# Performance work log

Hardware: AMD Instinct MI355X
Metric: run time of the kernel (lower is better)

The kernel has to match this reference:

```python
import jax, jax.numpy as jnp
import numpy as np

N = 50000
E = 800000
IN_C, HID_C, OUT_C = 5, 64, 32


def setup_inputs() -> dict:
    key = jax.random.key(0)
    ks = jax.random.split(key, 9)
    x = jax.random.normal(ks[0], (N, IN_C), dtype=jnp.float32)
    edge_index = jax.random.randint(ks[1], (2, E), 0, N, dtype=jnp.int64)
    # SAGEConv params: lin_l (neighbor path, has bias), lin_r (root path, no bias)
    def lin(k, fan_out, fan_in):
        s = 1.0 / np.sqrt(fan_in)
        return jax.random.uniform(k, (fan_out, fan_in), jnp.float32, -s, s)
    W1l = lin(ks[2], HID_C, IN_C); b1 = jnp.zeros((HID_C,), jnp.float32); W1r = lin(ks[3], HID_C, IN_C)
    W2l = lin(ks[4], HID_C, HID_C); b2 = jnp.zeros((HID_C,), jnp.float32); W2r = lin(ks[5], HID_C, HID_C)
    W3l = lin(ks[6], OUT_C, HID_C); b3 = jnp.zeros((OUT_C,), jnp.float32); W3r = lin(ks[7], OUT_C, HID_C)
    return {"x": x, "edge_index": edge_index,
            "W1l": W1l, "b1": b1, "W1r": W1r,
            "W2l": W2l, "b2": b2, "W2r": W2r,
            "W3l": W3l, "b3": b3, "W3r": W3r}


def _sage_conv(x, src, dst, inv_deg, Wl, bl, Wr):
    # PyG SAGEConv (aggr='mean'): out = lin_l(mean_j x_j) + lin_r(x)
    msg = x[src]                                          # [E, d_in] gather
    agg = jax.ops.segment_sum(msg, dst, num_segments=N)   # [N, d_in] scatter-add
    mean = agg * inv_deg                                  # mean aggregation
    return mean @ Wl.T + bl + x @ Wr.T


def reference(x, edge_index, W1l, b1, W1r, W2l, b2, W2r, W3l, b3, W3r):
    src, dst = edge_index[0], edge_index[1]
    deg = jax.ops.segment_sum(jnp.ones((E,), x.dtype), dst, num_segments=N)
    inv_deg = (1.0 / jnp.maximum(deg, 1.0))[:, None]      # [N, 1]
    h = jax.nn.relu(_sage_conv(x, src, dst, inv_deg, W1l, b1, W1r))
    # F.dropout(p=0.2, training=self.training): identity in eval mode
    h = jax.nn.relu(_sage_conv(h, src, dst, inv_deg, W2l, b2, W2r))
    out = _sage_conv(h, src, dst, inv_deg, W3l, b3, W3r)
    return out
```

## Files before the change

kernel.cpp:

```cpp
#include <hip/hip_runtime.h>
#include <hip/hip_fp16.h>


#define N_NODES 50000
#define N_EDGES 800000
#define IN_C 5
#define HID_C 64
#define OUT_C 32

#define NB 196
#define BCAP 6144
#define BWG 800
#define BCH (N_EDGES / BWG)

typedef __attribute__((ext_vector_type(8))) short bf16x8;
typedef __attribute__((ext_vector_type(4))) float f32x4;

__device__ __forceinline__ int rfl(int v) { return __builtin_amdgcn_readfirstlane(v); }
__device__ __forceinline__ float lanebc(float v, int l) {
    return __int_as_float(__builtin_amdgcn_readlane(__float_as_int(v), l));
}
__device__ __forceinline__ unsigned short f2bf(float f) {
    unsigned u = __float_as_uint(f);
    return (unsigned short)((u + 0x7fffu + ((u >> 16) & 1u)) >> 16);
}
__device__ __forceinline__ float bf2f(unsigned short b) {
    return __uint_as_float(((unsigned)b) << 16);
}
__device__ __forceinline__ float2 unpk_h2(unsigned u) {
    __half2 h = *(__half2*)&u;
    return __half22float2(h);
}


__global__ __launch_bounds__(256) void k_prep(
    const float* __restrict__ W2l, const float* __restrict__ W2r,
    const float* __restrict__ W3l, const float* __restrict__ W3r,
    unsigned short* __restrict__ W2hi, unsigned short* __restrict__ W2lo,
    unsigned short* __restrict__ W3zhi, unsigned short* __restrict__ W3zlo,
    int* __restrict__ gcur) {
    if (blockIdx.x == 0 && threadIdx.x < NB) gcur[threadIdx.x] = 0;
    const int t = blockIdx.x * 256 + threadIdx.x;
    const int stride = gridDim.x * 256;
    for (int p = t; p < 64 * 128; p += stride) {
        int j = p >> 7, k = p & 127;
        float w = (k < 64) ? W2l[j * 64 + k] : W2r[j * 64 + (k - 64)];
        unsigned short h = f2bf(w);
        W2hi[p] = h;
        W2lo[p] = f2bf(w - bf2f(h));
    }
    for (int p = t; p < 64 * 64; p += stride) {
        int j = p >> 6, k = p & 63;
        float w = (j < 32) ? W3l[j * 64 + k] : W3r[(j - 32) * 64 + k];
        unsigned short h = f2bf(w);
        W3zhi[p] = h;
        W3zlo[p] = f2bf(w - bf2f(h));
    }
}


__global__ __launch_bounds__(256) void k_bucket(const int* __restrict__ ei,
                                                int* __restrict__ gcur,
                                                unsigned* __restrict__ ebuf) {
    __shared__ int hist[NB];
    __shared__ int loff[NB];
    __shared__ int cur[NB];
    __shared__ int gbase[NB];
    __shared__ int scanb[256];
    __shared__ unsigned ev0[BCH];
    __shared__ unsigned stage[BCH];
    const int t = threadIdx.x;
    const int c0 = blockIdx.x * BCH;

    if (t < NB) hist[t] = 0;
    __syncthreads();
    for (int i = t; i < BCH; i += 256) {
        int s = ei[c0 + i];
        int d = ei[N_EDGES + c0 + i];
        ev0[i] = ((unsigned)d << 16) | (unsigned)s;
        atomicAdd(&hist[d >> 8], 1);
    }
    __syncthreads();
    scanb[t] = (t < NB) ? hist[t] : 0;
    __syncthreads();
#pragma unroll
    for (int o = 1; o < 256; o <<= 1) {
        int v = scanb[t];
        int a = (t >= o) ? scanb[t - o] : 0;
        __syncthreads();
        scanb[t] = v + a;
        __syncthreads();
    }
    if (t < NB) {
        int ex = (t == 0) ? 0 : scanb[t - 1];
        loff[t] = ex;
        cur[t] = ex;
        gbase[t] = atomicAdd(&gcur[t], hist[t]);
    }
    __syncthreads();
    for (int i = t; i < BCH; i += 256) {
        unsigned ev = ev0[i];
        int b = ev >> 24;
        int p = atomicAdd(&cur[b], 1);
        stage[p] = ev;
    }
    __syncthreads();
    for (int i = t; i < BCH; i += 256) {
        unsigned ev = stage[i];
        int b = ev >> 24;
        int pos = gbase[b] + (i - loff[b]);
        if (pos < BCAP) ebuf[b * BCAP + pos] = ev;
    }
}

__global__ __launch_bounds__(256) void k_bsort(const int* __restrict__ gcur,
                                               const unsigned* __restrict__ ebuf,
                                               int* __restrict__ row_off,
                                               float* __restrict__ inv_deg,
                                               int* __restrict__ srcs) {
    __shared__ int sc[256];
    __shared__ int cnt[256];
    __shared__ int loff[256];
    __shared__ int cur[256];
    __shared__ int stage[BCAP];
    const int t = threadIdx.x;
    const int b = blockIdx.x;

    sc[t] = (t < NB) ? gcur[t] : 0;
    __syncthreads();
#pragma unroll
    for (int o = 1; o < 256; o <<= 1) {
        int v = sc[t];
        int a = (t >= o) ? sc[t - o] : 0;
        __syncthreads();
        sc[t] = v + a;
        __syncthreads();
    }
    const int base = (b == 0) ? 0 : sc[b - 1];
    const int nraw = gcur[b];
    const int n = nraw < BCAP ? nraw : BCAP;
    const int node0 = b << 8;
    const unsigned* eb = ebuf + b * BCAP;

    cnt[t] = 0;
    __syncthreads();
    for (int i = t; i < n; i += 256) atomicAdd(&cnt[(eb[i] >> 16) & 255], 1);
    __syncthreads();
    loff[t] = cnt[t];
    __syncthreads();
#pragma unroll
    for (int o = 1; o < 256; o <<= 1) {
        int v = loff[t];
        int a = (t >= o) ? loff[t - o] : 0;
        __syncthreads();
        loff[t] = v + a;
        __syncthreads();
    }
    int ex = loff[t] - cnt[t];
    cur[t] = ex;
    int node = node0 + t;
    if (node < N_NODES) {
        row_off[node] = base + ex;
        int d = cnt[t];
        inv_deg[node] = 1.0f / (float)(d > 1 ? d : 1);
    }
    if (b == 0 && t == 0) row_off[N_NODES] = N_EDGES;
    __syncthreads();
    for (int i = t; i < n; i += 256) {
        unsigned ev = eb[i];
        int p = atomicAdd(&cur[(ev >> 16) & 255], 1);
        stage[p] = (int)(ev & 0xFFFFu);
    }
    __syncthreads();
    for (int i = t; i < n; i += 256) srcs[base + i] = stage[i];
}


__global__ __launch_bounds__(256) void k_layer1(
    const float* __restrict__ x, const int* __restrict__ row_off,
    const int* __restrict__ srcs, const float* __restrict__ inv_deg,
    const float* __restrict__ W1l, const float* __restrict__ b1,
    const float* __restrict__ W1r, __half* __restrict__ h1) {
    const int t = threadIdx.x;
    const int lane = t & 63;
    const int v = blockIdx.x * 4 + (t >> 6);
    if (v >= N_NODES) return;
    const int sub = lane >> 3;
    const int c = lane & 7;

    float wl[IN_C], wr[IN_C];
#pragma unroll
    for (int i = 0; i < IN_C; ++i) {
        wl[i] = W1l[lane * IN_C + i];
        wr[i] = W1r[lane * IN_C + i];
    }
    float bb = b1[lane];

    int beg = rfl(row_off[v]);
    int end = rfl(row_off[v + 1]);
    float xv = (lane < IN_C) ? x[v * IN_C + lane] : 0.f;
    float idg = inv_deg[v];
    float sum = 0.f;
    for (int e = beg; e < end; e += 8) {
        int o = e + sub;
        if (o < end && c < IN_C) sum += x[srcs[o] * IN_C + c];
    }
    sum += __shfl_xor(sum, 8, 64);
    sum += __shfl_xor(sum, 16, 64);
    sum += __shfl_xor(sum, 32, 64);
    float summ = sum * idg;
    float acc = bb;
#pragma unroll
    for (int i = 0; i < IN_C; ++i) {
        acc += wl[i] * lanebc(summ, i);
        acc += wr[i] * lanebc(xv, i);
    }
    h1[v * HID_C + lane] = __float2half(fmaxf(acc, 0.f));
}


__global__ __launch_bounds__(256) void k_fused2(
    const __half* __restrict__ h, const int* __restrict__ row_off,
    const int* __restrict__ srcs, const float* __restrict__ inv_deg,
    const unsigned short* __restrict__ W2hi, const unsigned short* __restrict__ W2lo,
    const float* __restrict__ b2,
    const unsigned short* __restrict__ W3zhi, const unsigned short* __restrict__ W3zlo,
    const float* __restrict__ b3,
    __half* __restrict__ z3l, float* __restrict__ z3r) {
    constexpr int AP = 152;
    __shared__ __align__(16) unsigned short Ah[32][AP];
    __shared__ __align__(16) unsigned short Al[32][AP];
    const int t = threadIdx.x;
    const int lane = t & 63;
    const int w = t >> 6;
    const int ns = lane >> 3;
    const int cg = lane & 7;
    const int node0 = blockIdx.x * 32;
    const int m = w * 8 + ns;
    const int v = node0 + m;
    const bool valid = v < N_NODES;
    const uint4* h4 = (const uint4*)h;

    int beg = 0, deg = 0;
    float idg = 0.f;
    uint4 ur = make_uint4(0u, 0u, 0u, 0u);
    if (valid) {
        beg = row_off[v];
        deg = row_off[v + 1] - beg;
        idg = inv_deg[v];
        ur = h4[v * 8 + cg];
    }

    const int* sp = srcs + beg;
    const int last = (deg > 0) ? (deg - 1) : 0;
#define SIDX(K) sp[(K) < last ? (K) : last]
    int j0 = SIDX(0), j1 = SIDX(1), j2 = SIDX(2), j3 = SIDX(3);
    int j4 = SIDX(4), j5 = SIDX(5), j6 = SIDX(6), j7 = SIDX(7);

    float s0 = 0.f, s1 = 0.f, s2 = 0.f, s3 = 0.f;
    float s4 = 0.f, s5 = 0.f, s6 = 0.f, s7 = 0.f;
    for (int k = 0; k < deg; k += 8) {
        uint4 u0 = h4[j0 * 8 + cg];
        uint4 u1 = h4[j1 * 8 + cg];
        uint4 u2 = h4[j2 * 8 + cg];
        uint4 u3 = h4[j3 * 8 + cg];
        uint4 u4 = h4[j4 * 8 + cg];
        uint4 u5 = h4[j5 * 8 + cg];
        uint4 u6 = h4[j6 * 8 + cg];
        uint4 u7 = h4[j7 * 8 + cg];
        float w1 = (k + 1 < deg) ? 1.f : 0.f;
        float w2 = (k + 2 < deg) ? 1.f : 0.f;
        float w3 = (k + 3 < deg) ? 1.f : 0.f;
        float w4 = (k + 4 < deg) ? 1.f : 0.f;
        float w5 = (k + 5 < deg) ? 1.f : 0.f;
        float w6 = (k + 6 < deg) ? 1.f : 0.f;
        float w7 = (k + 7 < deg) ? 1.f : 0.f;
        j0 = SIDX(k + 8);  j1 = SIDX(k + 9);  j2 = SIDX(k + 10); j3 = SIDX(k + 11);
        j4 = SIDX(k + 12); j5 = SIDX(k + 13); j6 = SIDX(k + 14); j7 = SIDX(k + 15);
        {
            float2 a = unpk_h2(u0.x), b = unpk_h2(u0.y);
            float2 c = unpk_h2(u0.z), d = unpk_h2(u0.w);
            s0 += a.x; s1 += a.y; s2 += b.x; s3 += b.y;
            s4 += c.x; s5 += c.y; s6 += d.x; s7 += d.y;
        }
#define ACCW(U, W)                                                     \
        {                                                              \
            float2 a = unpk_h2(U.x), b = unpk_h2(U.y);                 \
            float2 c = unpk_h2(U.z), d = unpk_h2(U.w);                 \
            s0 = fmaf(a.x, W, s0); s1 = fmaf(a.y, W, s1);              \
            s2 = fmaf(b.x, W, s2); s3 = fmaf(b.y, W, s3);              \
            s4 = fmaf(c.x, W, s4); s5 = fmaf(c.y, W, s5);              \
            s6 = fmaf(d.x, W, s6); s7 = fmaf(d.y, W, s7);              \
        }
        ACCW(u1, w1) ACCW(u2, w2) ACCW(u3, w3)
        ACCW(u4, w4) ACCW(u5, w5) ACCW(u6, w6) ACCW(u7, w7)
#undef ACCW
    }
#undef SIDX

    float m0 = s0 * idg, m1 = s1 * idg, m2 = s2 * idg, m3 = s3 * idg;
    float m4 = s4 * idg, m5 = s5 * idg, m6 = s6 * idg, m7 = s7 * idg;

    {
        unsigned short a0 = f2bf(m0), a1 = f2bf(m1), a2 = f2bf(m2), a3 = f2bf(m3);
        unsigned short a4 = f2bf(m4), a5 = f2bf(m5), a6 = f2bf(m6), a7 = f2bf(m7);
        uint4 hi, lo;
        hi.x = (unsigned)a0 | ((unsigned)a1 << 16);
        hi.y = (unsigned)a2 | ((unsigned)a3 << 16);
        hi.z = (unsigned)a4 | ((unsigned)a5 << 16);
        hi.w = (unsigned)a6 | ((unsigned)a7 << 16);
        lo.x = (unsigned)f2bf(m0 - bf2f(a0)) | ((unsigned)f2bf(m1 - bf2f(a1)) << 16);
        lo.y = (unsigned)f2bf(m2 - bf2f(a2)) | ((unsigned)f2bf(m3 - bf2f(a3)) << 16);
        lo.z = (unsigned)f2bf(m4 - bf2f(a4)) | ((unsigned)f2bf(m5 - bf2f(a5)) << 16);
        lo.w = (unsigned)f2bf(m6 - bf2f(a6)) | ((unsigned)f2bf(m7 - bf2f(a7)) << 16);
        *(uint4*)&Ah[m][cg * 8] = hi;
        *(uint4*)&Al[m][cg * 8] = lo;
    }
    {
        float2 p0 = unpk_h2(ur.x), p1 = unpk_h2(ur.y);
        float2 p2 = unpk_h2(ur.z), p3 = unpk_h2(ur.w);
        unsigned short a0 = f2bf(p0.x), a1 = f2bf(p0.y), a2 = f2bf(p1.x), a3 = f2bf(p1.y);
        unsigned short a4 = f2bf(p2.x), a5 = f2bf(p2.y), a6 = f2bf(p3.x), a7 = f2bf(p3.y);
        uint4 hi, lo;
        hi.x = (unsigned)a0 | ((unsigned)a1 << 16);
        hi.y = (unsigned)a2 | ((unsigned)a3 << 16);
        hi.z = (unsigned)a4 | ((unsigned)a5 << 16);
        hi.w = (unsigned)a6 | ((unsigned)a7 << 16);
        lo.x = (unsigned)f2bf(p0.x - bf2f(a0)) | ((unsigned)f2bf(p0.y - bf2f(a1)) << 16);
        lo.y = (unsigned)f2bf(p1.x - bf2f(a2)) | ((unsigned)f2bf(p1.y - bf2f(a3)) << 16);
        lo.z = (unsigned)f2bf(p2.x - bf2f(a4)) | ((unsigned)f2bf(p2.y - bf2f(a5)) << 16);
        lo.w = (unsigned)f2bf(p3.x - bf2f(a6)) | ((unsigned)f2bf(p3.y - bf2f(a7)) << 16);
        *(uint4*)&Ah[m][64 + cg * 8] = hi;
        *(uint4*)&Al[m][64 + cg * 8] = lo;
    }
    __syncthreads();

    const int r = lane & 15;
    const int quad = lane >> 4;
    f32x4 accA = (f32x4){0.f, 0.f, 0.f, 0.f};
    f32x4 accB = (f32x4){0.f, 0.f, 0.f, 0.f};
#pragma unroll
    for (int ks = 0; ks < 4; ++ks) {
        bf16x8 ah0 = *(const bf16x8*)&Ah[r][ks * 32 + quad * 8];
        bf16x8 al0 = *(const bf16x8*)&Al[r][ks * 32 + quad * 8];
        bf16x8 ah1 = *(const bf16x8*)&Ah[16 + r][ks * 32 + quad * 8];
        bf16x8 al1 = *(const bf16x8*)&Al[16 + r][ks * 32 + quad * 8];
        const size_t wb = ((size_t)(w * 16 + r)) * 128 + ks * 32 + quad * 8;
        bf16x8 bh = *(const bf16x8*)(W2hi + wb);
        bf16x8 bl = *(const bf16x8*)(W2lo + wb);
        accA = __builtin_amdgcn_mfma_f32_16x16x32_bf16(ah0, bh, accA, 0, 0, 0);
        accA = __builtin_amdgcn_mfma_f32_16x16x32_bf16(ah0, bl, accA, 0, 0, 0);
        accA = __builtin_amdgcn_mfma_f32_16x16x32_bf16(al0, bh, accA, 0, 0, 0);
        accB = __builtin_amdgcn_mfma_f32_16x16x32_bf16(ah1, bh, accB, 0, 0, 0);
        accB = __builtin_amdgcn_mfma_f32_16x16x32_bf16(ah1, bl, accB, 0, 0, 0);
        accB = __builtin_amdgcn_mfma_f32_16x16x32_bf16(al1, bh, accB, 0, 0, 0);
    }
    const float bv2 = b2[w * 16 + r];
    float h2A[4], h2B[4];
#pragma unroll
    for (int g = 0; g < 4; ++g) {
        h2A[g] = fmaxf(accA[g] + bv2, 0.f);
        h2B[g] = fmaxf(accB[g] + bv2, 0.f);
    }
    __syncthreads();

#pragma unroll
    for (int g = 0; g < 4; ++g) {
        unsigned short hiA = f2bf(h2A[g]);
        Ah[quad * 4 + g][w * 16 + r] = hiA;
        Al[quad * 4 + g][w * 16 + r] = f2bf(h2A[g] - bf2f(hiA));
        unsigned short hiB = f2bf(h2B[g]);
        Ah[16 + quad * 4 + g][w * 16 + r] = hiB;
        Al[16 + quad * 4 + g][w * 16 + r] = f2bf(h2B[g] - bf2f(hiB));
    }
    __syncthreads();

    f32x4 zA = (f32x4){0.f, 0.f, 0.f, 0.f};
    f32x4 zB = (f32x4){0.f, 0.f, 0.f, 0.f};
#pragma unroll
    for (int ks = 0; ks < 2; ++ks) {
        bf16x8 ah0 = *(const bf16x8*)&Ah[r][ks * 32 + quad * 8];
        bf16x8 al0 = *(const bf16x8*)&Al[r][ks * 32 + quad * 8];
        bf16x8 ah1 = *(const bf16x8*)&Ah[16 + r][ks * 32 + quad * 8];
        bf16x8 al1 = *(const bf16x8*)&Al[16 + r][ks * 32 + quad * 8];
        const size_t wb = ((size_t)(w * 16 + r)) * 64 + ks * 32 + quad * 8;
        bf16x8 bh = *(const bf16x8*)(W3zhi + wb);
        bf16x8 bl = *(const bf16x8*)(W3zlo + wb);
        zA = __builtin_amdgcn_mfma_f32_16x16x32_bf16(ah0, bh, zA, 0, 0, 0);
        zA = __builtin_amdgcn_mfma_f32_16x16x32_bf16(ah0, bl, zA, 0, 0, 0);
        zA = __builtin_amdgcn_mfma_f32_16x16x32_bf16(al0, bh, zA, 0, 0, 0);
        zB = __builtin_amdgcn_mfma_f32_16x16x32_bf16(ah1, bh, zB, 0, 0, 0);
        zB = __builtin_amdgcn_mfma_f32_16x16x32_bf16(ah1, bl, zB, 0, 0, 0);
        zB = __builtin_amdgcn_mfma_f32_16x16x32_bf16(al1, bh, zB, 0, 0, 0);
    }
    const int j = w * 16 + r;
    const float badd = (j >= 32) ? b3[j - 32] : 0.f;
#pragma unroll
    for (int g = 0; g < 4; ++g) {
        int nodeA = node0 + quad * 4 + g;
        int nodeB = node0 + 16 + quad * 4 + g;
        float vA = zA[g] + badd;
        float vB = zB[g] + badd;
        if (nodeA < N_NODES) {
            if (j < 32) z3l[(size_t)nodeA * 32 + j] = __float2half(vA);
            else        z3r[(size_t)nodeA * 32 + (j - 32)] = vA;
        }
        if (nodeB < N_NODES) {
            if (j < 32) z3l[(size_t)nodeB * 32 + j] = __float2half(vB);
            else        z3r[(size_t)nodeB * 32 + (j - 32)] = vB;
        }
    }
}


__global__ __launch_bounds__(256) void k_agg3(
    const int* __restrict__ row_off, const int* __restrict__ srcs,
    const float* __restrict__ inv_deg,
    const __half* __restrict__ z3l, const float* __restrict__ z3r,
    float* __restrict__ out) {
    const int t = threadIdx.x;
    const int lane = t & 63;
    const int v = blockIdx.x * 4 + (t >> 6);
    if (v >= N_NODES) return;
    const int slot = lane >> 2;
    const int cg = lane & 3;

    const int beg = rfl(row_off[v]);
    const int end = rfl(row_off[v + 1]);
    const int deg = end - beg;
    const float idg = inv_deg[v];
    const uint4* z4 = (const uint4*)z3l;

    float s0 = 0.f, s1 = 0.f, s2 = 0.f, s3 = 0.f;
    float s4 = 0.f, s5 = 0.f, s6 = 0.f, s7 = 0.f;
    for (int k = 0; k < deg; k += 16) {
        int o = beg + k + slot;
        int oc = (o < end) ? o : (end - 1);
        int jn = srcs[oc];
        uint4 u = z4[jn * 4 + cg];
        float wk = (k + slot < deg) ? 1.f : 0.f;
        float2 a = unpk_h2(u.x), b = unpk_h2(u.y);
        float2 c = unpk_h2(u.z), d = unpk_h2(u.w);
        s0 = fmaf(a.x, wk, s0); s1 = fmaf(a.y, wk, s1);
        s2 = fmaf(b.x, wk, s2); s3 = fmaf(b.y, wk, s3);
        s4 = fmaf(c.x, wk, s4); s5 = fmaf(c.y, wk, s5);
        s6 = fmaf(d.x, wk, s6); s7 = fmaf(d.y, wk, s7);
    }
#pragma unroll
    for (int off = 4; off <= 32; off <<= 1) {
        s0 += __shfl_xor(s0, off, 64); s1 += __shfl_xor(s1, off, 64);
        s2 += __shfl_xor(s2, off, 64); s3 += __shfl_xor(s3, off, 64);
        s4 += __shfl_xor(s4, off, 64); s5 += __shfl_xor(s5, off, 64);
        s6 += __shfl_xor(s6, off, 64); s7 += __shfl_xor(s7, off, 64);
    }
    if (lane < 4) {
        const float4* zr4 = (const float4*)(z3r + (size_t)v * 32);
        float4 r0 = zr4[lane * 2];
        float4 r1 = zr4[lane * 2 + 1];
        float4 o0, o1;
        o0.x = fmaf(s0, idg, r0.x); o0.y = fmaf(s1, idg, r0.y);
        o0.z = fmaf(s2, idg, r0.z); o0.w = fmaf(s3, idg, r0.w);
        o1.x = fmaf(s4, idg, r1.x); o1.y = fmaf(s5, idg, r1.y);
        o1.z = fmaf(s6, idg, r1.z); o1.w = fmaf(s7, idg, r1.w);
        float4* op = (float4*)(out + (size_t)v * 32);
        op[lane * 2] = o0;
        op[lane * 2 + 1] = o1;
    }
}


extern "C" void kernel_launch(void* const* d_in, const int* in_sizes, int n_in,
                              void* d_out, int out_size, void* d_ws, size_t ws_size,
                              hipStream_t stream) {
    const float* x   = (const float*)d_in[0];
    const int*   ei  = (const int*)d_in[1];
    const float* W1l = (const float*)d_in[2];
    const float* b1  = (const float*)d_in[3];
    const float* W1r = (const float*)d_in[4];
    const float* W2l = (const float*)d_in[5];
    const float* b2  = (const float*)d_in[6];
    const float* W2r = (const float*)d_in[7];
    const float* W3l = (const float*)d_in[8];
    const float* b3  = (const float*)d_in[9];
    const float* W3r = (const float*)d_in[10];

    char* ws = (char*)d_ws;
    size_t off = 0;
    auto alloc = [&](size_t bytes) -> char* {
        char* p = ws + off;
        off += (bytes + 255) & ~(size_t)255;
        return p;
    };
    int*      gcur   = (int*)alloc(NB * sizeof(int));
    int*      rowoff = (int*)alloc((N_NODES + 1) * sizeof(int));
    float*    invdeg = (float*)alloc(N_NODES * sizeof(float));
    int*      srcs   = (int*)alloc(N_EDGES * sizeof(int));
    unsigned* ebuf   = (unsigned*)alloc((size_t)NB * BCAP * sizeof(unsigned));
    __half*   h1     = (__half*)alloc((size_t)N_NODES * HID_C * sizeof(__half));
    __half*   z3l    = (__half*)alloc((size_t)N_NODES * OUT_C * sizeof(__half));
    float*    z3r    = (float*)alloc((size_t)N_NODES * OUT_C * sizeof(float));
    unsigned short* W2hi  = (unsigned short*)alloc(64 * 128 * 2);
    unsigned short* W2lo  = (unsigned short*)alloc(64 * 128 * 2);
    unsigned short* W3zhi = (unsigned short*)alloc(64 * 64 * 2);
    unsigned short* W3zlo = (unsigned short*)alloc(64 * 64 * 2);

    k_prep<<<dim3(48), dim3(256), 0, stream>>>(W2l, W2r, W3l, W3r,
                                               W2hi, W2lo, W3zhi, W3zlo, gcur);
    k_bucket<<<dim3(BWG), dim3(256), 0, stream>>>(ei, gcur, ebuf);
    k_bsort<<<dim3(NB), dim3(256), 0, stream>>>(gcur, ebuf, rowoff, invdeg, srcs);

    k_layer1<<<dim3(N_NODES / 4), dim3(256), 0, stream>>>(
        x, rowoff, srcs, invdeg, W1l, b1, W1r, h1);

    const int FT = (N_NODES + 31) / 32;
    k_fused2<<<dim3(FT), dim3(256), 0, stream>>>(
        h1, rowoff, srcs, invdeg, W2hi, W2lo, b2, W3zhi, W3zlo, b3, z3l, z3r);

    k_agg3<<<dim3((N_NODES + 3) / 4), dim3(256), 0, stream>>>(
        rowoff, srcs, invdeg, z3l, z3r, (float*)d_out);
}
```

Measured before the change: 178.4 us.

## Fuse weight prep into bucketing and layer-1 into bucket sort kernel

Merges the weight-splitting prep kernel into the edge bucketing kernel as extra blocks. It also folds layer 1 into the bucket-sort kernel, reusing the sorted neighbor lists already held in shared memory, with one thread computing all 64 outputs of a node. gcur is now zeroed with a memset. This drops kernel launches and the global re-read of srcs and row_off. The cost is that layer 1 runs on only 196 blocks with serial per-thread neighbor loops, so parallelism is much lower.

```diff
diff --git a/kernel.cpp b/kernel.cpp
--- a/kernel.cpp
+++ b/kernel.cpp
@@ -12,14 +12,12 @@
 #define BCAP 6144
 #define BWG 800
 #define BCH (N_EDGES / BWG)
+#define WPB 48
 
 typedef __attribute__((ext_vector_type(8))) short bf16x8;
 typedef __attribute__((ext_vector_type(4))) float f32x4;
 
 __device__ __forceinline__ int rfl(int v) { return __builtin_amdgcn_readfirstlane(v); }
-__device__ __forceinline__ float lanebc(float v, int l) {
-    return __int_as_float(__builtin_amdgcn_readlane(__float_as_int(v), l));
-}
 __device__ __forceinline__ unsigned short f2bf(float f) {
     unsigned u = __float_as_uint(f);
     return (unsigned short)((u + 0x7fffu + ((u >> 16) & 1u)) >> 16);
@@ -33,35 +31,32 @@
 }
 
 
-__global__ __launch_bounds__(256) void k_prep(
+__global__ __launch_bounds__(256) void k_bucketprep(
+    const int* __restrict__ ei, int* __restrict__ gcur,
+    unsigned* __restrict__ ebuf,
     const float* __restrict__ W2l, const float* __restrict__ W2r,
     const float* __restrict__ W3l, const float* __restrict__ W3r,
     unsigned short* __restrict__ W2hi, unsigned short* __restrict__ W2lo,
-    unsigned short* __restrict__ W3zhi, unsigned short* __restrict__ W3zlo,
-    int* __restrict__ gcur) {
-    if (blockIdx.x == 0 && threadIdx.x < NB) gcur[threadIdx.x] = 0;
-    const int t = blockIdx.x * 256 + threadIdx.x;
-    const int stride = gridDim.x * 256;
-    for (int p = t; p < 64 * 128; p += stride) {
-        int j = p >> 7, k = p & 127;
-        float w = (k < 64) ? W2l[j * 64 + k] : W2r[j * 64 + (k - 64)];
-        unsigned short h = f2bf(w);
-        W2hi[p] = h;
-        W2lo[p] = f2bf(w - bf2f(h));
-    }
-    for (int p = t; p < 64 * 64; p += stride) {
-        int j = p >> 6, k = p & 63;
-        float w = (j < 32) ? W3l[j * 64 + k] : W3r[(j - 32) * 64 + k];
-        unsigned short h = f2bf(w);
-        W3zhi[p] = h;
-        W3zlo[p] = f2bf(w - bf2f(h));
-    }
-}
-
-
-__global__ __launch_bounds__(256) void k_bucket(const int* __restrict__ ei,
-                                                int* __restrict__ gcur,
-                                                unsigned* __restrict__ ebuf) {
+    unsigned short* __restrict__ W3zhi, unsigned short* __restrict__ W3zlo) {
+    if (blockIdx.x >= BWG) {
+        const int t = (blockIdx.x - BWG) * 256 + threadIdx.x;
+        const int stride = WPB * 256;
+        for (int p = t; p < 64 * 128; p += stride) {
+            int j = p >> 7, k = p & 127;
+            float w = (k < 64) ? W2l[j * 64 + k] : W2r[j * 64 + (k - 64)];
+            unsigned short h = f2bf(w);
+            W2hi[p] = h;
+            W2lo[p] = f2bf(w - bf2f(h));
+        }
+        for (int p = t; p < 64 * 64; p += stride) {
+            int j = p >> 6, k = p & 63;
+            float w = (j < 32) ? W3l[j * 64 + k] : W3r[(j - 32) * 64 + k];
+            unsigned short h = f2bf(w);
+            W3zhi[p] = h;
+            W3zlo[p] = f2bf(w - bf2f(h));
+        }
+        return;
+    }
     __shared__ int hist[NB];
     __shared__ int loff[NB];
     __shared__ int cur[NB];
@@ -113,18 +108,30 @@
     }
 }
 
-__global__ __launch_bounds__(256) void k_bsort(const int* __restrict__ gcur,
-                                               const unsigned* __restrict__ ebuf,
-                                               int* __restrict__ row_off,
-                                               float* __restrict__ inv_deg,
-                                               int* __restrict__ srcs) {
+
+__global__ __launch_bounds__(256) void k_bsort_l1(
+    const int* __restrict__ gcur, const unsigned* __restrict__ ebuf,
+    int* __restrict__ row_off, float* __restrict__ inv_deg,
+    int* __restrict__ srcs,
+    const float* __restrict__ x, const float* __restrict__ W1l,
+    const float* __restrict__ b1, const float* __restrict__ W1r,
+    __half* __restrict__ h1) {
     __shared__ int sc[256];
     __shared__ int cnt[256];
     __shared__ int loff[256];
     __shared__ int cur[256];
     __shared__ int stage[BCAP];
+    __shared__ float w1l[64 * IN_C];
+    __shared__ float w1r[64 * IN_C];
+    __shared__ float bb1[64];
     const int t = threadIdx.x;
     const int b = blockIdx.x;
+
+    for (int i = t; i < 64 * IN_C; i += 256) {
+        w1l[i] = W1l[i];
+        w1r[i] = W1r[i];
+    }
+    if (t < 64) bb1[t] = b1[t];
 
     sc[t] = (t < NB) ? gcur[t] : 0;
     __syncthreads();
@@ -156,13 +163,13 @@
         loff[t] = v + a;
         __syncthreads();
     }
-    int ex = loff[t] - cnt[t];
+    const int ex = loff[t] - cnt[t];
+    const int deg = cnt[t];
     cur[t] = ex;
-    int node = node0 + t;
+    const int node = node0 + t;
     if (node < N_NODES) {
         row_off[node] = base + ex;
-        int d = cnt[t];
-        inv_deg[node] = 1.0f / (float)(d > 1 ? d : 1);
+        inv_deg[node] = 1.0f / (float)(deg > 1 ? deg : 1);
     }
     if (b == 0 && t == 0) row_off[N_NODES] = N_EDGES;
     __syncthreads();
@@ -173,49 +180,46 @@
     }
     __syncthreads();
     for (int i = t; i < n; i += 256) srcs[base + i] = stage[i];
-}
-
-
-__global__ __launch_bounds__(256) void k_layer1(
-    const float* __restrict__ x, const int* __restrict__ row_off,
-    const int* __restrict__ srcs, const float* __restrict__ inv_deg,
-    const float* __restrict__ W1l, const float* __restrict__ b1,
-    const float* __restrict__ W1r, __half* __restrict__ h1) {
-    const int t = threadIdx.x;
-    const int lane = t & 63;
-    const int v = blockIdx.x * 4 + (t >> 6);
-    if (v >= N_NODES) return;
-    const int sub = lane >> 3;
-    const int c = lane & 7;
-
-    float wl[IN_C], wr[IN_C];
-#pragma unroll
-    for (int i = 0; i < IN_C; ++i) {
-        wl[i] = W1l[lane * IN_C + i];
-        wr[i] = W1r[lane * IN_C + i];
-    }
-    float bb = b1[lane];
-
-    int beg = rfl(row_off[v]);
-    int end = rfl(row_off[v + 1]);
-    float xv = (lane < IN_C) ? x[v * IN_C + lane] : 0.f;
-    float idg = inv_deg[v];
-    float sum = 0.f;
-    for (int e = beg; e < end; e += 8) {
-        int o = e + sub;
-        if (o < end && c < IN_C) sum += x[srcs[o] * IN_C + c];
-    }
-    sum += __shfl_xor(sum, 8, 64);
-    sum += __shfl_xor(sum, 16, 64);
-    sum += __shfl_xor(sum, 32, 64);
-    float summ = sum * idg;
-    float acc = bb;
-#pragma unroll
-    for (int i = 0; i < IN_C; ++i) {
-        acc += wl[i] * lanebc(summ, i);
-        acc += wr[i] * lanebc(xv, i);
-    }
-    h1[v * HID_C + lane] = __float2half(fmaxf(acc, 0.f));
+
+    if (node >= N_NODES) return;
+    float mm[IN_C] = {0.f, 0.f, 0.f, 0.f, 0.f};
+    for (int i = 0; i < deg; ++i) {
+        int j = stage[ex + i];
+        const float* xp = x + j * IN_C;
+#pragma unroll
+        for (int q = 0; q < IN_C; ++q) mm[q] += xp[q];
+    }
+    const float idg = 1.0f / (float)(deg > 1 ? deg : 1);
+#pragma unroll
+    for (int q = 0; q < IN_C; ++q) mm[q] *= idg;
+    float rr[IN_C];
+    const float* xr = x + (size_t)node * IN_C;
+#pragma unroll
+    for (int q = 0; q < IN_C; ++q) rr[q] = xr[q];
+
+    uint4* hrow = (uint4*)(h1 + (size_t)node * HID_C);
+#pragma unroll
+    for (int ob = 0; ob < 8; ++ob) {
+        float oc[8];
+#pragma unroll
+        for (int q = 0; q < 8; ++q) {
+            const int o = ob * 8 + q;
+            float acc = bb1[o];
+#pragma unroll
+            for (int i = 0; i < IN_C; ++i) {
+                acc = fmaf(w1l[o * IN_C + i], mm[i], acc);
+                acc = fmaf(w1r[o * IN_C + i], rr[i], acc);
+            }
+            oc[q] = fmaxf(acc, 0.f);
+        }
+        unsigned uu[4];
+#pragma unroll
+        for (int q = 0; q < 4; ++q) {
+            __half2 hh = __floats2half2_rn(oc[2 * q], oc[2 * q + 1]);
+            uu[q] = *reinterpret_cast<unsigned*>(&hh);
+        }
+        hrow[ob] = make_uint4(uu[0], uu[1], uu[2], uu[3]);
+    }
 }
 
 
@@ -504,13 +508,13 @@
     unsigned short* W3zhi = (unsigned short*)alloc(64 * 64 * 2);
     unsigned short* W3zlo = (unsigned short*)alloc(64 * 64 * 2);
 
-    k_prep<<<dim3(48), dim3(256), 0, stream>>>(W2l, W2r, W3l, W3r,
-                                               W2hi, W2lo, W3zhi, W3zlo, gcur);
-    k_bucket<<<dim3(BWG), dim3(256), 0, stream>>>(ei, gcur, ebuf);
-    k_bsort<<<dim3(NB), dim3(256), 0, stream>>>(gcur, ebuf, rowoff, invdeg, srcs);
-
-    k_layer1<<<dim3(N_NODES / 4), dim3(256), 0, stream>>>(
-        x, rowoff, srcs, invdeg, W1l, b1, W1r, h1);
+    hipMemsetAsync(gcur, 0, NB * sizeof(int), stream);
+
+    k_bucketprep<<<dim3(BWG + WPB), dim3(256), 0, stream>>>(
+        ei, gcur, ebuf, W2l, W2r, W3l, W3r, W2hi, W2lo, W3zhi, W3zlo);
+
+    k_bsort_l1<<<dim3(NB), dim3(256), 0, stream>>>(
+        gcur, ebuf, rowoff, invdeg, srcs, x, W1l, b1, W1r, h1);
 
     const int FT = (N_NODES + 31) / 32;
     k_fused2<<<dim3(FT), dim3(256), 0, stream>>>(
```

Measured after the change: 165.1 us. -7.5%, faster.

## Replace two-pass bucket-sort CSR build with atomic per-node fixed-slot adjacency lists

Applied to the files above, without the earlier changes.

Drops the two-kernel bucketed counting sort that built row offsets and sorted source lists. In its place, one kernel scatters each edge's source into a fixed 64-entry slot array per destination node, using an atomic degree counter. The weight-prep work moves into extra blocks of that same kernel, and a memset clears the degree counters. All consumers now read degree and slots directly and compute the inverse degree on the fly, which removes the scans and extra launches. The cost is a larger, sparsely filled adjacency buffer, and any node with more than 64 incoming edges has its neighbours silently truncated.

```diff
diff --git a/kernel.cpp b/kernel.cpp
--- a/kernel.cpp
+++ b/kernel.cpp
@@ -8,15 +8,13 @@
 #define HID_C 64
 #define OUT_C 32
 
-#define NB 196
-#define BCAP 6144
-#define BWG 800
-#define BCH (N_EDGES / BWG)
+#define SLOT 64
+#define SCB 1600
+#define WPB 48
 
 typedef __attribute__((ext_vector_type(8))) short bf16x8;
 typedef __attribute__((ext_vector_type(4))) float f32x4;
 
-__device__ __forceinline__ int rfl(int v) { return __builtin_amdgcn_readfirstlane(v); }
 __device__ __forceinline__ float lanebc(float v, int l) {
     return __int_as_float(__builtin_amdgcn_readlane(__float_as_int(v), l));
 }
@@ -33,152 +31,46 @@
 }
 
 
-__global__ __launch_bounds__(256) void k_prep(
+__global__ __launch_bounds__(256) void k_scatterprep(
+    const int* __restrict__ ei, int* __restrict__ deg,
+    int* __restrict__ slots,
     const float* __restrict__ W2l, const float* __restrict__ W2r,
     const float* __restrict__ W3l, const float* __restrict__ W3r,
     unsigned short* __restrict__ W2hi, unsigned short* __restrict__ W2lo,
-    unsigned short* __restrict__ W3zhi, unsigned short* __restrict__ W3zlo,
-    int* __restrict__ gcur) {
-    if (blockIdx.x == 0 && threadIdx.x < NB) gcur[threadIdx.x] = 0;
+    unsigned short* __restrict__ W3zhi, unsigned short* __restrict__ W3zlo) {
+    if (blockIdx.x >= SCB) {
+        const int t = (blockIdx.x - SCB) * 256 + threadIdx.x;
+        const int stride = WPB * 256;
+        for (int p = t; p < 64 * 128; p += stride) {
+            int j = p >> 7, k = p & 127;
+            float w = (k < 64) ? W2l[j * 64 + k] : W2r[j * 64 + (k - 64)];
+            unsigned short h = f2bf(w);
+            W2hi[p] = h;
+            W2lo[p] = f2bf(w - bf2f(h));
+        }
+        for (int p = t; p < 64 * 64; p += stride) {
+            int j = p >> 6, k = p & 63;
+            float w = (j < 32) ? W3l[j * 64 + k] : W3r[(j - 32) * 64 + k];
+            unsigned short h = f2bf(w);
+            W3zhi[p] = h;
+            W3zlo[p] = f2bf(w - bf2f(h));
+        }
+        return;
+    }
     const int t = blockIdx.x * 256 + threadIdx.x;
-    const int stride = gridDim.x * 256;
-    for (int p = t; p < 64 * 128; p += stride) {
-        int j = p >> 7, k = p & 127;
-        float w = (k < 64) ? W2l[j * 64 + k] : W2r[j * 64 + (k - 64)];
-        unsigned short h = f2bf(w);
-        W2hi[p] = h;
-        W2lo[p] = f2bf(w - bf2f(h));
-    }
-    for (int p = t; p < 64 * 64; p += stride) {
-        int j = p >> 6, k = p & 63;
-        float w = (j < 32) ? W3l[j * 64 + k] : W3r[(j - 32) * 64 + k];
-        unsigned short h = f2bf(w);
-        W3zhi[p] = h;
-        W3zlo[p] = f2bf(w - bf2f(h));
-    }
-}
-
-
-__global__ __launch_bounds__(256) void k_bucket(const int* __restrict__ ei,
-                                                int* __restrict__ gcur,
-                                                unsigned* __restrict__ ebuf) {
-    __shared__ int hist[NB];
-    __shared__ int loff[NB];
-    __shared__ int cur[NB];
-    __shared__ int gbase[NB];
-    __shared__ int scanb[256];
-    __shared__ unsigned ev0[BCH];
-    __shared__ unsigned stage[BCH];
-    const int t = threadIdx.x;
-    const int c0 = blockIdx.x * BCH;
-
-    if (t < NB) hist[t] = 0;
-    __syncthreads();
-    for (int i = t; i < BCH; i += 256) {
-        int s = ei[c0 + i];
-        int d = ei[N_EDGES + c0 + i];
-        ev0[i] = ((unsigned)d << 16) | (unsigned)s;
-        atomicAdd(&hist[d >> 8], 1);
-    }
-    __syncthreads();
-    scanb[t] = (t < NB) ? hist[t] : 0;
-    __syncthreads();
-#pragma unroll
-    for (int o = 1; o < 256; o <<= 1) {
-        int v = scanb[t];
-        int a = (t >= o) ? scanb[t - o] : 0;
-        __syncthreads();
-        scanb[t] = v + a;
-        __syncthreads();
-    }
-    if (t < NB) {
-        int ex = (t == 0) ? 0 : scanb[t - 1];
-        loff[t] = ex;
-        cur[t] = ex;
-        gbase[t] = atomicAdd(&gcur[t], hist[t]);
-    }
-    __syncthreads();
-    for (int i = t; i < BCH; i += 256) {
-        unsigned ev = ev0[i];
-        int b = ev >> 24;
-        int p = atomicAdd(&cur[b], 1);
-        stage[p] = ev;
-    }
-    __syncthreads();
-    for (int i = t; i < BCH; i += 256) {
-        unsigned ev = stage[i];
-        int b = ev >> 24;
-        int pos = gbase[b] + (i - loff[b]);
-        if (pos < BCAP) ebuf[b * BCAP + pos] = ev;
-    }
-}
-
-__global__ __launch_bounds__(256) void k_bsort(const int* __restrict__ gcur,
-                                               const unsigned* __restrict__ ebuf,
-                                               int* __restrict__ row_off,
-                                               float* __restrict__ inv_deg,
-                                               int* __restrict__ srcs) {
-    __shared__ int sc[256];
-    __shared__ int cnt[256];
-    __shared__ int loff[256];
-    __shared__ int cur[256];
-    __shared__ int stage[BCAP];
-    const int t = threadIdx.x;
-    const int b = blockIdx.x;
-
-    sc[t] = (t < NB) ? gcur[t] : 0;
-    __syncthreads();
-#pragma unroll
-    for (int o = 1; o < 256; o <<= 1) {
-        int v = sc[t];
-        int a = (t >= o) ? sc[t - o] : 0;
-        __syncthreads();
-        sc[t] = v + a;
-        __syncthreads();
-    }
-    const int base = (b == 0) ? 0 : sc[b - 1];
-    const int nraw = gcur[b];
-    const int n = nraw < BCAP ? nraw : BCAP;
-    const int node0 = b << 8;
-    const unsigned* eb = ebuf + b * BCAP;
-
-    cnt[t] = 0;
-    __syncthreads();
-    for (int i = t; i < n; i += 256) atomicAdd(&cnt[(eb[i] >> 16) & 255], 1);
-    __syncthreads();
-    loff[t] = cnt[t];
-    __syncthreads();
-#pragma unroll
-    for (int o = 1; o < 256; o <<= 1) {
-        int v = loff[t];
-        int a = (t >= o) ? loff[t - o] : 0;
-        __syncthreads();
-        loff[t] = v + a;
-        __syncthreads();
-    }
-    int ex = loff[t] - cnt[t];
-    cur[t] = ex;
-    int node = node0 + t;
-    if (node < N_NODES) {
-        row_off[node] = base + ex;
-        int d = cnt[t];
-        inv_deg[node] = 1.0f / (float)(d > 1 ? d : 1);
-    }
-    if (b == 0 && t == 0) row_off[N_NODES] = N_EDGES;
-    __syncthreads();
-    for (int i = t; i < n; i += 256) {
-        unsigned ev = eb[i];
-        int p = atomicAdd(&cur[(ev >> 16) & 255], 1);
-        stage[p] = (int)(ev & 0xFFFFu);
-    }
-    __syncthreads();
-    for (int i = t; i < n; i += 256) srcs[base + i] = stage[i];
-}
-
-
-__global__ __launch_bounds__(256) void k_layer1(
-    const float* __restrict__ x, const int* __restrict__ row_off,
-    const int* __restrict__ srcs, const float* __restrict__ inv_deg,
+    const int stride = SCB * 256;
+    for (int i = t; i < N_EDGES; i += stride) {
+        int s = ei[i];
+        int d = ei[N_EDGES + i];
+        int pos = atomicAdd(&deg[d], 1);
+        if (pos < SLOT) slots[(size_t)d * SLOT + pos] = s;
+    }
+}
+
+
+__global__ __launch_bounds__(256) void k_l1(
+    const float* __restrict__ x, const int* __restrict__ deg,
+    const int* __restrict__ slots,
     const float* __restrict__ W1l, const float* __restrict__ b1,
     const float* __restrict__ W1r, __half* __restrict__ h1) {
     const int t = threadIdx.x;
@@ -196,14 +88,15 @@
     }
     float bb = b1[lane];
 
-    int beg = rfl(row_off[v]);
-    int end = rfl(row_off[v + 1]);
+    int d = deg[v];
+    if (d > SLOT) d = SLOT;
+    const float idg = 1.0f / (float)(d > 1 ? d : 1);
+    const int* sp = slots + (size_t)v * SLOT;
     float xv = (lane < IN_C) ? x[v * IN_C + lane] : 0.f;
-    float idg = inv_deg[v];
     float sum = 0.f;
-    for (int e = beg; e < end; e += 8) {
+    for (int e = 0; e < d; e += 8) {
         int o = e + sub;
-        if (o < end && c < IN_C) sum += x[srcs[o] * IN_C + c];
+        if (o < d && c < IN_C) sum += x[sp[o] * IN_C + c];
     }
     sum += __shfl_xor(sum, 8, 64);
     sum += __shfl_xor(sum, 16, 64);
@@ -220,8 +113,8 @@
 
 
 __global__ __launch_bounds__(256) void k_fused2(
-    const __half* __restrict__ h, const int* __restrict__ row_off,
-    const int* __restrict__ srcs, const float* __restrict__ inv_deg,
+    const __half* __restrict__ h, const int* __restrict__ deg,
+    const int* __restrict__ slots,
     const unsigned short* __restrict__ W2hi, const unsigned short* __restrict__ W2lo,
     const float* __restrict__ b2,
     const unsigned short* __restrict__ W3zhi, const unsigned short* __restrict__ W3zlo,
@@ -241,25 +134,25 @@
     const bool valid = v < N_NODES;
     const uint4* h4 = (const uint4*)h;
 
-    int beg = 0, deg = 0;
+    int dg = 0;
     float idg = 0.f;
     uint4 ur = make_uint4(0u, 0u, 0u, 0u);
     if (valid) {
-        beg = row_off[v];
-        deg = row_off[v + 1] - beg;
-        idg = inv_deg[v];
+        dg = deg[v];
+        if (dg > SLOT) dg = SLOT;
+        idg = 1.0f / (float)(dg > 1 ? dg : 1);
         ur = h4[v * 8 + cg];
     }
 
-    const int* sp = srcs + beg;
-    const int last = (deg > 0) ? (deg - 1) : 0;
+    const int* sp = slots + (size_t)(valid ? v : 0) * SLOT;
+    const int last = (dg > 0) ? (dg - 1) : 0;
 #define SIDX(K) sp[(K) < last ? (K) : last]
     int j0 = SIDX(0), j1 = SIDX(1), j2 = SIDX(2), j3 = SIDX(3);
     int j4 = SIDX(4), j5 = SIDX(5), j6 = SIDX(6), j7 = SIDX(7);
 
     float s0 = 0.f, s1 = 0.f, s2 = 0.f, s3 = 0.f;
     float s4 = 0.f, s5 = 0.f, s6 = 0.f, s7 = 0.f;
-    for (int k = 0; k < deg; k += 8) {
+    for (int k = 0; k < dg; k += 8) {
         uint4 u0 = h4[j0 * 8 + cg];
         uint4 u1 = h4[j1 * 8 + cg];
         uint4 u2 = h4[j2 * 8 + cg];
@@ -268,13 +161,13 @@
         uint4 u5 = h4[j5 * 8 + cg];
         uint4 u6 = h4[j6 * 8 + cg];
         uint4 u7 = h4[j7 * 8 + cg];
-        float w1 = (k + 1 < deg) ? 1.f : 0.f;
-        float w2 = (k + 2 < deg) ? 1.f : 0.f;
-        float w3 = (k + 3 < deg) ? 1.f : 0.f;
-        float w4 = (k + 4 < deg) ? 1.f : 0.f;
-        float w5 = (k + 5 < deg) ? 1.f : 0.f;
-        float w6 = (k + 6 < deg) ? 1.f : 0.f;
-        float w7 = (k + 7 < deg) ? 1.f : 0.f;
+        float w1 = (k + 1 < dg) ? 1.f : 0.f;
+        float w2 = (k + 2 < dg) ? 1.f : 0.f;
+        float w3 = (k + 3 < dg) ? 1.f : 0.f;
+        float w4 = (k + 4 < dg) ? 1.f : 0.f;
+        float w5 = (k + 5 < dg) ? 1.f : 0.f;
+        float w6 = (k + 6 < dg) ? 1.f : 0.f;
+        float w7 = (k + 7 < dg) ? 1.f : 0.f;
         j0 = SIDX(k + 8);  j1 = SIDX(k + 9);  j2 = SIDX(k + 10); j3 = SIDX(k + 11);
         j4 = SIDX(k + 12); j5 = SIDX(k + 13); j6 = SIDX(k + 14); j7 = SIDX(k + 15);
         {
@@ -414,8 +307,7 @@
 
 
 __global__ __launch_bounds__(256) void k_agg3(
-    const int* __restrict__ row_off, const int* __restrict__ srcs,
-    const float* __restrict__ inv_deg,
+    const int* __restrict__ deg, const int* __restrict__ slots,
     const __half* __restrict__ z3l, const float* __restrict__ z3r,
     float* __restrict__ out) {
     const int t = threadIdx.x;
@@ -425,26 +317,27 @@
     const int slot = lane >> 2;
     const int cg = lane & 3;
 
-    const int beg = rfl(row_off[v]);
-    const int end = rfl(row_off[v + 1]);
-    const int deg = end - beg;
-    const float idg = inv_deg[v];
+    int d = deg[v];
+    if (d > SLOT) d = SLOT;
+    const float idg = 1.0f / (float)(d > 1 ? d : 1);
+    const int* sp = slots + (size_t)v * SLOT;
     const uint4* z4 = (const uint4*)z3l;
 
     float s0 = 0.f, s1 = 0.f, s2 = 0.f, s3 = 0.f;
     float s4 = 0.f, s5 = 0.f, s6 = 0.f, s7 = 0.f;
-    for (int k = 0; k < deg; k += 16) {
-        int o = beg + k + slot;
-        int oc = (o < end) ? o : (end - 1);
-        int jn = srcs[oc];
+    for (int k = 0; k < d; k += 16) {
+        int o = k + slot;
+        int oc = (o < d) ? o : (d - 1);
+        if (oc < 0) oc = 0;
+        int jn = sp[oc];
         uint4 u = z4[jn * 4 + cg];
-        float wk = (k + slot < deg) ? 1.f : 0.f;
+        float wk = (o < d) ? 1.f : 0.f;
         float2 a = unpk_h2(u.x), b = unpk_h2(u.y);
-        float2 c = unpk_h2(u.z), d = unpk_h2(u.w);
+        float2 c = unpk_h2(u.z), dd = unpk_h2(u.w);
         s0 = fmaf(a.x, wk, s0); s1 = fmaf(a.y, wk, s1);
         s2 = fmaf(b.x, wk, s2); s3 = fmaf(b.y, wk, s3);
         s4 = fmaf(c.x, wk, s4); s5 = fmaf(c.y, wk, s5);
-        s6 = fmaf(d.x, wk, s6); s7 = fmaf(d.y, wk, s7);
+        s6 = fmaf(dd.x, wk, s6); s7 = fmaf(dd.y, wk, s7);
     }
 #pragma unroll
     for (int off = 4; off <= 32; off <<= 1) {
@@ -491,11 +384,8 @@
         off += (bytes + 255) & ~(size_t)255;
         return p;
     };
-    int*      gcur   = (int*)alloc(NB * sizeof(int));
-    int*      rowoff = (int*)alloc((N_NODES + 1) * sizeof(int));
-    float*    invdeg = (float*)alloc(N_NODES * sizeof(float));
-    int*      srcs   = (int*)alloc(N_EDGES * sizeof(int));
-    unsigned* ebuf   = (unsigned*)alloc((size_t)NB * BCAP * sizeof(unsigned));
+    int*      deg    = (int*)alloc(N_NODES * sizeof(int));
+    int*      slots  = (int*)alloc((size_t)N_NODES * SLOT * sizeof(int));
     __half*   h1     = (__half*)alloc((size_t)N_NODES * HID_C * sizeof(__half));
     __half*   z3l    = (__half*)alloc((size_t)N_NODES * OUT_C * sizeof(__half));
     float*    z3r    = (float*)alloc((size_t)N_NODES * OUT_C * sizeof(float));
@@ -504,18 +394,18 @@
     unsigned short* W3zhi = (unsigned short*)alloc(64 * 64 * 2);
     unsigned short* W3zlo = (unsigned short*)alloc(64 * 64 * 2);
 
-    k_prep<<<dim3(48), dim3(256), 0, stream>>>(W2l, W2r, W3l, W3r,
-                                               W2hi, W2lo, W3zhi, W3zlo, gcur);
-    k_bucket<<<dim3(BWG), dim3(256), 0, stream>>>(ei, gcur, ebuf);
-    k_bsort<<<dim3(NB), dim3(256), 0, stream>>>(gcur, ebuf, rowoff, invdeg, srcs);
-
-    k_layer1<<<dim3(N_NODES / 4), dim3(256), 0, stream>>>(
-        x, rowoff, srcs, invdeg, W1l, b1, W1r, h1);
+    hipMemsetAsync(deg, 0, N_NODES * sizeof(int), stream);
+
+    k_scatterprep<<<dim3(SCB + WPB), dim3(256), 0, stream>>>(
+        ei, deg, slots, W2l, W2r, W3l, W3r, W2hi, W2lo, W3zhi, W3zlo);
+
+    k_l1<<<dim3((N_NODES + 3) / 4), dim3(256), 0, stream>>>(
+        x, deg, slots, W1l, b1, W1r, h1);
 
     const int FT = (N_NODES + 31) / 32;
     k_fused2<<<dim3(FT), dim3(256), 0, stream>>>(
-        h1, rowoff, srcs, invdeg, W2hi, W2lo, b2, W3zhi, W3zlo, b3, z3l, z3r);
+        h1, deg, slots, W2hi, W2lo, b2, W3zhi, W3zlo, b3, z3l, z3r);
 
     k_agg3<<<dim3((N_NODES + 3) / 4), dim3(256), 0, stream>>>(
-        rowoff, srcs, invdeg, z3l, z3r, (float*)d_out);
-}
+        deg, slots, z3l, z3r, (float*)d_out);
+}
```

Measured after the change: 197.8 us. +10.9%, slower.
